# Performance work log

Measured on AMD Instinct MI355X. Metric: run time of the kernel, lower is better.

The kernel has to match this reference:

```python
import jax, jax.numpy as jnp
import numpy as np

N_NODES = 50000
N_EDGES = 800000
IN_FEATS, N_HIDDEN, N_CLASSES = 128, 128, 64
N_LAYERS = 3  # total GraphConv layers = N_LAYERS + 1


def setup_inputs() -> dict:
    key = jax.random.key(0)
    ks = jax.random.split(key, 16)
    features = jax.random.normal(ks[0], (N_NODES, IN_FEATS), dtype=jnp.float32)
    src = jax.random.randint(ks[1], (N_EDGES,), 0, N_NODES, dtype=jnp.int32)
    dst = jax.random.randint(ks[2], (N_EDGES,), 0, N_NODES, dtype=jnp.int32)
    def lin(k, fan_in, fan_out):
        s = 1.0 / np.sqrt(fan_in)
        return jax.random.uniform(k, (fan_in, fan_out), jnp.float32, -s, s)
    dims = [IN_FEATS] + [N_HIDDEN] * N_LAYERS + [N_CLASSES]
    inp = {"features": features, "src": src, "dst": dst}
    for i in range(len(dims) - 1):
        inp[f"W{i}"] = lin(ks[3 + i], dims[i], dims[i + 1])
        inp[f"b{i}"] = jnp.zeros((dims[i + 1],), jnp.float32)
    inp["Wp"] = lin(ks[10], N_CLASSES, 1)
    inp["bp"] = jnp.zeros((1,), jnp.float32)
    inp["Wv"] = lin(ks[11], N_CLASSES, 1)
    inp["bv"] = jnp.zeros((1,), jnp.float32)
    return inp


def _graph_conv(h, src, dst, norm_src, norm_dst, W, b, activate):
    # DGL GraphConv, norm='both': D_out^{-1/2} A D_in^{-1/2} X W + b
    h = h * norm_src  # [N, d]
    msg = h[src]      # [E, d] gather
    agg = jax.ops.segment_sum(msg, dst, num_segments=N_NODES)  # [N, d] scatter-add
    out = agg * norm_dst @ W + b
    return jax.nn.relu(out) if activate else out


def reference(features, src, dst, W0, b0, W1, b1, W2, b2, W3, b3, Wp, bp, Wv, bv):
    ones = jnp.ones((N_EDGES,), jnp.float32)
    out_deg = jax.ops.segment_sum(ones, src, num_segments=N_NODES)
    in_deg = jax.ops.segment_sum(ones, dst, num_segments=N_NODES)
    norm_src = jnp.clip(out_deg, 1.0) ** -0.5  # [N]
    norm_dst = jnp.clip(in_deg, 1.0) ** -0.5
    norm_src = norm_src[:, None]
    norm_dst = norm_dst[:, None]
    Ws = [W0, W1, W2, W3]
    bs = [b0, b1, b2, b3]
    h = features
    for i in range(4):
        h = _graph_conv(h, src, dst, norm_src, norm_dst, Ws[i], bs[i], activate=(i < 3))
    mN = jnp.sum(h, axis=0, keepdims=True)  # readout_nodes sum -> [1, n_classes]
    PI = h @ Wp + bp   # [N, 1]
    V = mN @ Wv + bv   # [1, 1]
    return (PI, V)
```

## Files before the change

### kernel.cpp

```cpp
#include <hip/hip_runtime.h>
#include <cstddef>

#define N_NODES 50000
#define N_EDGES 800000
#define NBUK    196
#define NBLK    256
#define EPB     3125
#define HEAD_BLOCKS 3136

typedef unsigned u32;
typedef unsigned short u16;
typedef unsigned char u8;
typedef __attribute__((ext_vector_type(8))) short bf16x8;
typedef __attribute__((ext_vector_type(4))) float f32x4;

__device__ __forceinline__ float bflo(u32 u) { return __uint_as_float(u << 16); }
__device__ __forceinline__ float bfhi(u32 u) { return __uint_as_float(u & 0xFFFF0000u); }
__device__ __forceinline__ u32 f2bf(float f) {
    u32 u = __float_as_uint(f);
    return (u + 0x7FFFu + ((u >> 16) & 1u)) >> 16;
}
__device__ __forceinline__ u32 packbf2(float a, float b) { return f2bf(a) | (f2bf(b) << 16); }

#define OFF_NS    0u
#define OFF_ND    200000u
#define OFF_RS    400000u
#define OFF_ES    600016u
#define OFF_CNTD  2200016u
#define OFF_CNTS  2400720u
#define OFF_TOTD  2601424u
#define OFF_TOTS  2602208u
#define OFF_BASED 2602992u
#define OFF_BASES 2603776u
#define OFF_VP    2604560u
#define OFF_DB    2617104u
#define OFF_SB    5817104u
#define OFF_T0    6617104u
#define OFF_T1    19417104u
#define OFF_TA    32217104u
#define OFF_TT    45017104u

__global__ __launch_bounds__(256)
void p1_kernel(const int* __restrict__ src, const int* __restrict__ dst,
               u32* __restrict__ cntD, u32* __restrict__ cntS) {
    __shared__ u32 dc[NBUK], sc[NBUK];
    int b = blockIdx.x, tid = threadIdx.x;
    if (tid < NBUK) { dc[tid] = 0; sc[tid] = 0; }
    __syncthreads();
    int lo = b * EPB, hi = lo + EPB;
    for (int e = lo + tid; e < hi; e += 256) {
        atomicAdd(&dc[dst[e] >> 8], 1u);
        atomicAdd(&sc[src[e] >> 8], 1u);
    }
    __syncthreads();
    if (tid < NBUK) {
        cntD[b * NBUK + tid] = dc[tid];
        cntS[b * NBUK + tid] = sc[tid];
    }
}

__global__ __launch_bounds__(256)
void p2a_kernel(u32* __restrict__ cntD, u32* __restrict__ cntS,
                u32* __restrict__ totD, u32* __restrict__ totS) {
    __shared__ u32 sc[256];
    int k = blockIdx.x, tid = threadIdx.x;
    u32 v = cntD[tid * NBUK + k];
    sc[tid] = v;
    __syncthreads();
    for (int o = 1; o < 256; o <<= 1) {
        u32 t = (tid >= o) ? sc[tid - o] : 0u;
        __syncthreads(); sc[tid] += t; __syncthreads();
    }
    cntD[tid * NBUK + k] = sc[tid] - v;
    if (tid == 255) totD[k] = sc[255];
    __syncthreads();
    v = cntS[tid * NBUK + k];
    sc[tid] = v;
    __syncthreads();
    for (int o = 1; o < 256; o <<= 1) {
        u32 t = (tid >= o) ? sc[tid - o] : 0u;
        __syncthreads(); sc[tid] += t; __syncthreads();
    }
    cntS[tid * NBUK + k] = sc[tid] - v;
    if (tid == 255) totS[k] = sc[255];
}

__global__ __launch_bounds__(256)
void p2b_kernel(const u32* __restrict__ totD, const u32* __restrict__ totS,
                u32* __restrict__ baseD, u32* __restrict__ baseS, u32* __restrict__ rs) {
    __shared__ u32 sc[256];
    int tid = threadIdx.x;
    u32 v = (tid < NBUK) ? totD[tid] : 0u;
    sc[tid] = v;
    __syncthreads();
    for (int o = 1; o < 256; o <<= 1) {
        u32 t = (tid >= o) ? sc[tid - o] : 0u;
        __syncthreads(); sc[tid] += t; __syncthreads();
    }
    if (tid < NBUK) baseD[tid] = sc[tid] - v;
    __syncthreads();
    v = (tid < NBUK) ? totS[tid] : 0u;
    sc[tid] = v;
    __syncthreads();
    for (int o = 1; o < 256; o <<= 1) {
        u32 t = (tid >= o) ? sc[tid - o] : 0u;
        __syncthreads(); sc[tid] += t; __syncthreads();
    }
    if (tid < NBUK) baseS[tid] = sc[tid] - v;
    if (tid == 0) rs[N_NODES] = N_EDGES;
}

__global__ __launch_bounds__(256)
void p3_kernel(const int* __restrict__ src, const int* __restrict__ dst,
               const u32* __restrict__ cntD, const u32* __restrict__ cntS,
               const u32* __restrict__ baseD, const u32* __restrict__ baseS,
               u32* __restrict__ db, u8* __restrict__ sb) {
    __shared__ u32 od[NBUK], os[NBUK];
    int b = blockIdx.x, tid = threadIdx.x;
    if (tid < NBUK) {
        od[tid] = baseD[tid] + cntD[b * NBUK + tid];
        os[tid] = baseS[tid] + cntS[b * NBUK + tid];
    }
    __syncthreads();
    int lo = b * EPB, hi = lo + EPB;
    for (int e = lo + tid; e < hi; e += 256) {
        int s = src[e], d = dst[e];
        u32 p = atomicAdd(&od[d >> 8], 1u);
        db[p] = ((u32)s << 8) | (u32)(d & 255);
        u32 q = atomicAdd(&os[s >> 8], 1u);
        sb[q] = (u8)(s & 255);
    }
}

__global__ __launch_bounds__(256)
void p4d_kernel(const u32* __restrict__ db, const u32* __restrict__ totD,
                const u32* __restrict__ baseD, float* __restrict__ nd,
                u32* __restrict__ rs, u16* __restrict__ es) {
    __shared__ u32 hist[256], sc[256], off[256];
    int k = blockIdx.x, tid = threadIdx.x;
    hist[tid] = 0;
    __syncthreads();
    u32 nEd = totD[k], base = baseD[k];
    for (u32 i = tid; i < nEd; i += 256)
        atomicAdd(&hist[db[base + i] & 255u], 1u);
    __syncthreads();
    u32 v = hist[tid];
    sc[tid] = v;
    __syncthreads();
    for (int o = 1; o < 256; o <<= 1) {
        u32 t = (tid >= o) ? sc[tid - o] : 0u;
        __syncthreads(); sc[tid] += t; __syncthreads();
    }
    u32 pf = sc[tid] - v;
    int node = k * 256 + tid;
    if (node < N_NODES) {
        rs[node] = base + pf;
        u32 c = v < 1u ? 1u : v;
        nd[node] = rsqrtf((float)c);
    }
    off[tid] = base + pf;
    __syncthreads();
    for (u32 i = tid; i < nEd; i += 256) {
        u32 p = db[base + i];
        u32 pos = atomicAdd(&off[p & 255u], 1u);
        es[pos] = (u16)(p >> 8);
    }
}

__global__ __launch_bounds__(256)
void p4sp_kernel(const u8* __restrict__ sb, const u32* __restrict__ totS,
                 const u32* __restrict__ baseS, float* __restrict__ ns,
                 const float* __restrict__ feat, u16* __restrict__ hS) {
    __shared__ u32 hist[256];
    __shared__ float sns[256];
    int k = blockIdx.x, tid = threadIdx.x;
    hist[tid] = 0;
    __syncthreads();
    u32 n = totS[k], base = baseS[k];
    for (u32 i = tid; i < n; i += 256)
        atomicAdd(&hist[sb[base + i]], 1u);
    __syncthreads();
    int node = k * 256 + tid;
    {
        u32 c = hist[tid]; if (c < 1u) c = 1u;
        float s = rsqrtf((float)c);
        sns[tid] = s;
        if (node < N_NODES) ns[node] = s;
    }
    __syncthreads();
    for (int i = tid; i < 256 * 32; i += 256) {
        int r = i >> 5, c4 = i & 31;
        int g = k * 256 + r;
        if (g >= N_NODES) break;
        float s = sns[r];
        float4 v = *(const float4*)&feat[(size_t)g * 128 + c4 * 4];
        uint2 o;
        o.x = packbf2(s * v.x, s * v.y);
        o.y = packbf2(s * v.z, s * v.w);
        *(uint2*)&hS[(size_t)g * 128 + c4 * 4] = o;
    }
}

__global__ __launch_bounds__(256)
void agg128_kernel(const u16* __restrict__ h, const u32* __restrict__ rs,
                   const u16* __restrict__ es, u16* __restrict__ agg) {
    int node = blockIdx.x * 4 + (threadIdx.x >> 6);
    int lane = threadIdx.x & 63;
    int quarter = lane >> 4;
    int q = lane & 15;
    const uint4* hp = (const uint4*)h;
    u32 s0 = rs[node], s1 = rs[node + 1];
    float acc[8] = {0.f, 0.f, 0.f, 0.f, 0.f, 0.f, 0.f, 0.f};
    u32 i = s0;
    for (; i + 16 <= s1; i += 16) {
        int e0 = es[i + quarter],     e1 = es[i + 4 + quarter];
        int e2 = es[i + 8 + quarter], e3 = es[i + 12 + quarter];
        uint4 a = hp[(size_t)e0 * 16 + q];
        uint4 b = hp[(size_t)e1 * 16 + q];
        uint4 c = hp[(size_t)e2 * 16 + q];
        uint4 d = hp[(size_t)e3 * 16 + q];
        acc[0] += (bflo(a.x) + bflo(b.x)) + (bflo(c.x) + bflo(d.x));
        acc[1] += (bfhi(a.x) + bfhi(b.x)) + (bfhi(c.x) + bfhi(d.x));
        acc[2] += (bflo(a.y) + bflo(b.y)) + (bflo(c.y) + bflo(d.y));
        acc[3] += (bfhi(a.y) + bfhi(b.y)) + (bfhi(c.y) + bfhi(d.y));
        acc[4] += (bflo(a.z) + bflo(b.z)) + (bflo(c.z) + bflo(d.z));
        acc[5] += (bfhi(a.z) + bfhi(b.z)) + (bfhi(c.z) + bfhi(d.z));
        acc[6] += (bflo(a.w) + bflo(b.w)) + (bflo(c.w) + bflo(d.w));
        acc[7] += (bfhi(a.w) + bfhi(b.w)) + (bfhi(c.w) + bfhi(d.w));
    }
    for (; i + 4 <= s1; i += 4) {
        uint4 a = hp[(size_t)es[i + quarter] * 16 + q];
        acc[0] += bflo(a.x); acc[1] += bfhi(a.x);
        acc[2] += bflo(a.y); acc[3] += bfhi(a.y);
        acc[4] += bflo(a.z); acc[5] += bfhi(a.z);
        acc[6] += bflo(a.w); acc[7] += bfhi(a.w);
    }
    u32 rem = s1 - i;
    if ((u32)quarter < rem) {
        uint4 a = hp[(size_t)es[i + quarter] * 16 + q];
        acc[0] += bflo(a.x); acc[1] += bfhi(a.x);
        acc[2] += bflo(a.y); acc[3] += bfhi(a.y);
        acc[4] += bflo(a.z); acc[5] += bfhi(a.z);
        acc[6] += bflo(a.w); acc[7] += bfhi(a.w);
    }
    #pragma unroll
    for (int j = 0; j < 8; ++j) {
        acc[j] += __shfl_xor(acc[j], 16, 64);
        acc[j] += __shfl_xor(acc[j], 32, 64);
    }
    if (lane < 16) {
        uint4 pk;
        pk.x = packbf2(acc[0], acc[1]);
        pk.y = packbf2(acc[2], acc[3]);
        pk.z = packbf2(acc[4], acc[5]);
        pk.w = packbf2(acc[6], acc[7]);
        *(uint4*)&agg[(size_t)node * 128 + q * 8] = pk;
    }
}

template <int NCOL, int MODE>
__global__ __launch_bounds__(256)
void mfma_gemm_kernel(const u16* __restrict__ Ab, const float* __restrict__ W,
                      const float* __restrict__ bias, const float* __restrict__ ns,
                      const float* __restrict__ nd, u16* __restrict__ C) {
    constexpr int NT = NCOL / 16;
    constexpr int WROW = 136;
    constexpr int CROW = NCOL + 4;
    __shared__ u16 Wt[NCOL * WROW];
    __shared__ float Cl[4][16 * CROW];
    int tid = threadIdx.x;
    int w = tid >> 6, lane = tid & 63;
    int rowbase = blockIdx.x * 64 + w * 16;

    for (int i = tid; i < 64 * NCOL; i += 256) {
        int k2 = i / NCOL, c = i % NCOL;
        float w0 = W[(size_t)(2 * k2) * NCOL + c];
        float w1 = W[(size_t)(2 * k2 + 1) * NCOL + c];
        *(u32*)&Wt[c * WROW + 2 * k2] = packbf2(w0, w1);
    }
    __syncthreads();

    int m = lane & 15, kb = lane >> 4;
    int arow = rowbase + m;
    if (arow > N_NODES - 1) arow = N_NODES - 1;
    f32x4 acc[NT];
    #pragma unroll
    for (int nt = 0; nt < NT; ++nt) acc[nt] = (f32x4){0.f, 0.f, 0.f, 0.f};

    #pragma unroll
    for (int ks = 0; ks < 4; ++ks) {
        int k0 = ks * 32 + kb * 8;
        bf16x8 a = *(const bf16x8*)&Ab[(size_t)arow * 128 + k0];
        #pragma unroll
        for (int nt = 0; nt < NT; ++nt) {
            bf16x8 b = *(const bf16x8*)&Wt[(nt * 16 + m) * WROW + k0];
            acc[nt] = __builtin_amdgcn_mfma_f32_16x16x32_bf16(a, b, acc[nt], 0, 0, 0);
        }
    }

    #pragma unroll
    for (int nt = 0; nt < NT; ++nt)
        #pragma unroll
        for (int reg = 0; reg < 4; ++reg)
            Cl[w][(kb * 4 + reg) * CROW + nt * 16 + m] = acc[nt][reg];
    __syncthreads();

    constexpr int CQ = NCOL / 4;
    for (int i = lane; i < 16 * CQ; i += 64) {
        int r = i / CQ, c4 = (i % CQ) * 4;
        int row = rowbase + r;
        if (row < N_NODES) {
            float4 o = *(float4*)&Cl[w][r * CROW + c4];
            if (MODE == 0) {
                float sd = nd[row], ss = ns[row];
                o.x = ss * fmaxf(sd * o.x + bias[c4 + 0], 0.f);
                o.y = ss * fmaxf(sd * o.y + bias[c4 + 1], 0.f);
                o.z = ss * fmaxf(sd * o.z + bias[c4 + 2], 0.f);
                o.w = ss * fmaxf(sd * o.w + bias[c4 + 3], 0.f);
            }
            uint2 pk = {packbf2(o.x, o.y), packbf2(o.z, o.w)};
            *(uint2*)&C[(size_t)row * NCOL + c4] = pk;
        }
    }
}

__global__ __launch_bounds__(256)
void l3head_kernel(const u16* __restrict__ t, const u32* __restrict__ rs,
                   const u16* __restrict__ es, const float* __restrict__ nd,
                   const float* __restrict__ b3, const float* __restrict__ Wp,
                   const float* __restrict__ Wv, const float* __restrict__ bp,
                   float* __restrict__ out, float* __restrict__ vpart) {
    __shared__ float sv;
    if (threadIdx.x == 0) sv = 0.f;
    __syncthreads();
    int lane = threadIdx.x & 63;
    int wvid = threadIdx.x >> 6;
    int oct = lane >> 3;
    int q = lane & 7;
    const uint4* hp = (const uint4*)t;
    float4 b3a = ((const float4*)b3)[q * 2];
    float4 b3b = ((const float4*)b3)[q * 2 + 1];
    float4 wpa = ((const float4*)Wp)[q * 2];
    float4 wpb = ((const float4*)Wp)[q * 2 + 1];
    float4 wva = ((const float4*)Wv)[q * 2];
    float4 wvb = ((const float4*)Wv)[q * 2 + 1];
    float bpv = bp[0];
    float vacc = 0.f;
    for (int n = blockIdx.x * 4 + wvid; n < N_NODES; n += HEAD_BLOCKS * 4) {
        u32 s0 = rs[n], s1 = rs[n + 1];
        float acc[8] = {0.f, 0.f, 0.f, 0.f, 0.f, 0.f, 0.f, 0.f};
        u32 i = s0;
        for (; i + 32 <= s1; i += 32) {
            int e0 = es[i + oct],      e1 = es[i + 8 + oct];
            int e2 = es[i + 16 + oct], e3 = es[i + 24 + oct];
            uint4 a = hp[(size_t)e0 * 8 + q];
            uint4 bb = hp[(size_t)e1 * 8 + q];
            uint4 c = hp[(size_t)e2 * 8 + q];
            uint4 d = hp[(size_t)e3 * 8 + q];
            acc[0] += (bflo(a.x) + bflo(bb.x)) + (bflo(c.x) + bflo(d.x));
            acc[1] += (bfhi(a.x) + bfhi(bb.x)) + (bfhi(c.x) + bfhi(d.x));
            acc[2] += (bflo(a.y) + bflo(bb.y)) + (bflo(c.y) + bflo(d.y));
            acc[3] += (bfhi(a.y) + bfhi(bb.y)) + (bfhi(c.y) + bfhi(d.y));
            acc[4] += (bflo(a.z) + bflo(bb.z)) + (bflo(c.z) + bflo(d.z));
            acc[5] += (bfhi(a.z) + bfhi(bb.z)) + (bfhi(c.z) + bfhi(d.z));
            acc[6] += (bflo(a.w) + bflo(bb.w)) + (bflo(c.w) + bflo(d.w));
            acc[7] += (bfhi(a.w) + bfhi(bb.w)) + (bfhi(c.w) + bfhi(d.w));
        }
        for (; i + 8 <= s1; i += 8) {
            uint4 a = hp[(size_t)es[i + oct] * 8 + q];
            acc[0] += bflo(a.x); acc[1] += bfhi(a.x);
            acc[2] += bflo(a.y); acc[3] += bfhi(a.y);
            acc[4] += bflo(a.z); acc[5] += bfhi(a.z);
            acc[6] += bflo(a.w); acc[7] += bfhi(a.w);
        }
        u32 rem = s1 - i;
        if ((u32)oct < rem) {
            uint4 a = hp[(size_t)es[i + oct] * 8 + q];
            acc[0] += bflo(a.x); acc[1] += bfhi(a.x);
            acc[2] += bflo(a.y); acc[3] += bfhi(a.y);
            acc[4] += bflo(a.z); acc[5] += bfhi(a.z);
            acc[6] += bflo(a.w); acc[7] += bfhi(a.w);
        }
        #pragma unroll
        for (int j = 0; j < 8; ++j) {
            acc[j] += __shfl_xor(acc[j], 8, 64);
            acc[j] += __shfl_xor(acc[j], 16, 64);
            acc[j] += __shfl_xor(acc[j], 32, 64);
        }
        float ndv = nd[n];
        float h0 = ndv * acc[0] + b3a.x, h1 = ndv * acc[1] + b3a.y;
        float h2 = ndv * acc[2] + b3a.z, h3 = ndv * acc[3] + b3a.w;
        float h4 = ndv * acc[4] + b3b.x, h5 = ndv * acc[5] + b3b.y;
        float h6 = ndv * acc[6] + b3b.z, h7 = ndv * acc[7] + b3b.w;
        float p  = h0 * wpa.x + h1 * wpa.y + h2 * wpa.z + h3 * wpa.w
                 + h4 * wpb.x + h5 * wpb.y + h6 * wpb.z + h7 * wpb.w;
        float vv = h0 * wva.x + h1 * wva.y + h2 * wva.z + h3 * wva.w
                 + h4 * wvb.x + h5 * wvb.y + h6 * wvb.z + h7 * wvb.w;
        p  += __shfl_xor(p, 1, 64);  p  += __shfl_xor(p, 2, 64);  p  += __shfl_xor(p, 4, 64);
        vv += __shfl_xor(vv, 1, 64); vv += __shfl_xor(vv, 2, 64); vv += __shfl_xor(vv, 4, 64);
        if (lane == 0) { out[n] = p + bpv; vacc += vv; }
    }
    if (lane == 0) atomicAdd(&sv, vacc);
    __syncthreads();
    if (threadIdx.x == 0) vpart[blockIdx.x] = sv;
}

__global__ __launch_bounds__(256)
void vred_kernel(const float* __restrict__ vpart, const float* __restrict__ bv,
                 float* __restrict__ out) {
    float v = 0.f;
    for (int i = threadIdx.x; i < HEAD_BLOCKS; i += 256) v += vpart[i];
    #pragma unroll
    for (int off = 32; off; off >>= 1) v += __shfl_down(v, off, 64);
    __shared__ float s[4];
    if ((threadIdx.x & 63) == 0) s[threadIdx.x >> 6] = v;
    __syncthreads();
    if (threadIdx.x == 0) out[N_NODES] = s[0] + s[1] + s[2] + s[3] + bv[0];
}

extern "C" void kernel_launch(void* const* d_in, const int* in_sizes, int n_in,
                              void* d_out, int out_size, void* d_ws, size_t ws_size,
                              hipStream_t stream) {
    const float* feat = (const float*)d_in[0];
    const int*   src  = (const int*)d_in[1];
    const int*   dst  = (const int*)d_in[2];
    const float* W0 = (const float*)d_in[3];  const float* b0 = (const float*)d_in[4];
    const float* W1 = (const float*)d_in[5];  const float* b1 = (const float*)d_in[6];
    const float* W2 = (const float*)d_in[7];  const float* b2 = (const float*)d_in[8];
    const float* W3 = (const float*)d_in[9];  const float* b3 = (const float*)d_in[10];
    const float* Wp = (const float*)d_in[11]; const float* bp = (const float*)d_in[12];
    const float* Wv = (const float*)d_in[13]; const float* bv = (const float*)d_in[14];
    float* out = (float*)d_out;
    char*  wsb = (char*)d_ws;

    float* ns    = (float*)(wsb + OFF_NS);
    float* nd    = (float*)(wsb + OFF_ND);
    u32*   rs    = (u32*)(wsb + OFF_RS);
    u16*   es    = (u16*)(wsb + OFF_ES);
    u32*   cntD  = (u32*)(wsb + OFF_CNTD);
    u32*   cntS  = (u32*)(wsb + OFF_CNTS);
    u32*   totD  = (u32*)(wsb + OFF_TOTD);
    u32*   totS  = (u32*)(wsb + OFF_TOTS);
    u32*   baseD = (u32*)(wsb + OFF_BASED);
    u32*   baseS = (u32*)(wsb + OFF_BASES);
    float* vpart = (float*)(wsb + OFF_VP);
    u32*   db    = (u32*)(wsb + OFF_DB);
    u8*    sb    = (u8*)(wsb + OFF_SB);
    u16*   T0    = (u16*)(wsb + OFF_T0);
    u16*   T1    = (u16*)(wsb + OFF_T1);
    u16*   TA    = (u16*)(wsb + OFF_TA);
    u16*   Tt    = (u16*)(wsb + OFF_TT);

    p1_kernel<<<NBLK, 256, 0, stream>>>(src, dst, cntD, cntS);
    p2a_kernel<<<NBUK, 256, 0, stream>>>(cntD, cntS, totD, totS);
    p2b_kernel<<<1, 256, 0, stream>>>(totD, totS, baseD, baseS, rs);
    p3_kernel<<<NBLK, 256, 0, stream>>>(src, dst, cntD, cntS, baseD, baseS, db, sb);
    p4d_kernel<<<NBUK, 256, 0, stream>>>(db, totD, baseD, nd, rs, es);
    p4sp_kernel<<<NBUK, 256, 0, stream>>>(sb, totS, baseS, ns, feat, T0);

    agg128_kernel<<<12500, 256, 0, stream>>>(T0, rs, es, TA);
    mfma_gemm_kernel<128, 0><<<782, 256, 0, stream>>>(TA, W0, b0, ns, nd, T1);
    agg128_kernel<<<12500, 256, 0, stream>>>(T1, rs, es, TA);
    mfma_gemm_kernel<128, 0><<<782, 256, 0, stream>>>(TA, W1, b1, ns, nd, T0);
    agg128_kernel<<<12500, 256, 0, stream>>>(T0, rs, es, TA);
    mfma_gemm_kernel<128, 0><<<782, 256, 0, stream>>>(TA, W2, b2, ns, nd, T1);
    mfma_gemm_kernel<64, 1><<<782, 256, 0, stream>>>(T1, W3, b3, ns, nd, Tt);
    l3head_kernel<<<HEAD_BLOCKS, 256, 0, stream>>>(Tt, rs, es, nd, b3, Wp, Wv, bp, out, vpart);
    vred_kernel<<<1, 256, 0, stream>>>(vpart, bv, out);
}
```

Measured before the change: 355.1 us.

## Fuse neighbor aggregation with MFMA GEMM and pre-convert weights once

Merges the per-layer aggregation and GEMM kernels into one kernel. Each block aggregates 32 node rows into shared memory and then multiplies them by the weights with MFMA. Weights are converted to bf16 and transposed once in a new upfront kernel and read straight from global memory, instead of being repacked into LDS by every GEMM block. This removes the bf16 round-trip of the aggregated tensor through global memory and three kernel launches. In exchange, each wave now processes 8 nodes serially, which lowers the parallelism available to hide gather latency, and every block re-reads the weight fragments from global/L2.

```diff
diff --git a/kernel.cpp b/kernel.cpp
--- a/kernel.cpp
+++ b/kernel.cpp
@@ -37,8 +37,9 @@
 #define OFF_SB    5817104u
 #define OFF_T0    6617104u
 #define OFF_T1    19417104u
-#define OFF_TA    32217104u
+#define OFF_T2    32217104u
 #define OFF_TT    45017104u
+#define OFF_WT    51417104u
 
 __global__ __launch_bounds__(256)
 void p1_kernel(const int* __restrict__ src, const int* __restrict__ dst,
@@ -202,124 +203,155 @@
 }
 
 __global__ __launch_bounds__(256)
-void agg128_kernel(const u16* __restrict__ h, const u32* __restrict__ rs,
-                   const u16* __restrict__ es, u16* __restrict__ agg) {
-    int node = blockIdx.x * 4 + (threadIdx.x >> 6);
-    int lane = threadIdx.x & 63;
-    int quarter = lane >> 4;
-    int q = lane & 15;
-    const uint4* hp = (const uint4*)h;
-    u32 s0 = rs[node], s1 = rs[node + 1];
-    float acc[8] = {0.f, 0.f, 0.f, 0.f, 0.f, 0.f, 0.f, 0.f};
-    u32 i = s0;
-    for (; i + 16 <= s1; i += 16) {
-        int e0 = es[i + quarter],     e1 = es[i + 4 + quarter];
-        int e2 = es[i + 8 + quarter], e3 = es[i + 12 + quarter];
-        uint4 a = hp[(size_t)e0 * 16 + q];
-        uint4 b = hp[(size_t)e1 * 16 + q];
-        uint4 c = hp[(size_t)e2 * 16 + q];
-        uint4 d = hp[(size_t)e3 * 16 + q];
-        acc[0] += (bflo(a.x) + bflo(b.x)) + (bflo(c.x) + bflo(d.x));
-        acc[1] += (bfhi(a.x) + bfhi(b.x)) + (bfhi(c.x) + bfhi(d.x));
-        acc[2] += (bflo(a.y) + bflo(b.y)) + (bflo(c.y) + bflo(d.y));
-        acc[3] += (bfhi(a.y) + bfhi(b.y)) + (bfhi(c.y) + bfhi(d.y));
-        acc[4] += (bflo(a.z) + bflo(b.z)) + (bflo(c.z) + bflo(d.z));
-        acc[5] += (bfhi(a.z) + bfhi(b.z)) + (bfhi(c.z) + bfhi(d.z));
-        acc[6] += (bflo(a.w) + bflo(b.w)) + (bflo(c.w) + bflo(d.w));
-        acc[7] += (bfhi(a.w) + bfhi(b.w)) + (bfhi(c.w) + bfhi(d.w));
-    }
-    for (; i + 4 <= s1; i += 4) {
-        uint4 a = hp[(size_t)es[i + quarter] * 16 + q];
-        acc[0] += bflo(a.x); acc[1] += bfhi(a.x);
-        acc[2] += bflo(a.y); acc[3] += bfhi(a.y);
-        acc[4] += bflo(a.z); acc[5] += bfhi(a.z);
-        acc[6] += bflo(a.w); acc[7] += bfhi(a.w);
-    }
-    u32 rem = s1 - i;
-    if ((u32)quarter < rem) {
-        uint4 a = hp[(size_t)es[i + quarter] * 16 + q];
-        acc[0] += bflo(a.x); acc[1] += bfhi(a.x);
-        acc[2] += bflo(a.y); acc[3] += bfhi(a.y);
-        acc[4] += bflo(a.z); acc[5] += bfhi(a.z);
-        acc[6] += bflo(a.w); acc[7] += bfhi(a.w);
-    }
-    #pragma unroll
-    for (int j = 0; j < 8; ++j) {
-        acc[j] += __shfl_xor(acc[j], 16, 64);
-        acc[j] += __shfl_xor(acc[j], 32, 64);
-    }
-    if (lane < 16) {
-        uint4 pk;
-        pk.x = packbf2(acc[0], acc[1]);
-        pk.y = packbf2(acc[2], acc[3]);
-        pk.z = packbf2(acc[4], acc[5]);
-        pk.w = packbf2(acc[6], acc[7]);
-        *(uint4*)&agg[(size_t)node * 128 + q * 8] = pk;
-    }
-}
-
-template <int NCOL, int MODE>
-__global__ __launch_bounds__(256)
-void mfma_gemm_kernel(const u16* __restrict__ Ab, const float* __restrict__ W,
-                      const float* __restrict__ bias, const float* __restrict__ ns,
-                      const float* __restrict__ nd, u16* __restrict__ C) {
-    constexpr int NT = NCOL / 16;
-    constexpr int WROW = 136;
-    constexpr int CROW = NCOL + 4;
-    __shared__ u16 Wt[NCOL * WROW];
-    __shared__ float Cl[4][16 * CROW];
+void wconv_kernel(const float* __restrict__ W0, const float* __restrict__ W1,
+                  const float* __restrict__ W2, const float* __restrict__ W3,
+                  u16* __restrict__ wt) {
+    int i = blockIdx.x * 256 + threadIdx.x;
+    if (i < 49152) {
+        int l = i / 16384, r = i % 16384;
+        int c = r >> 7, k = r & 127;
+        const float* W = (l == 0) ? W0 : (l == 1) ? W1 : W2;
+        wt[l * 16384 + r] = (u16)f2bf(W[k * 128 + c]);
+    } else if (i < 49152 + 8192) {
+        int r = i - 49152;
+        int c = r >> 7, k = r & 127;
+        wt[49152 + r] = (u16)f2bf(W3[k * 64 + c]);
+    }
+}
+
+__global__ __launch_bounds__(256)
+void aggmm_kernel(const u16* __restrict__ h, const u32* __restrict__ rs,
+                  const u16* __restrict__ es, const u16* __restrict__ wt,
+                  const float* __restrict__ bias, const float* __restrict__ ns,
+                  const float* __restrict__ nd, u16* __restrict__ C) {
+    __shared__ u16 As[32 * 136];
     int tid = threadIdx.x;
     int w = tid >> 6, lane = tid & 63;
-    int rowbase = blockIdx.x * 64 + w * 16;
-
-    for (int i = tid; i < 64 * NCOL; i += 256) {
-        int k2 = i / NCOL, c = i % NCOL;
-        float w0 = W[(size_t)(2 * k2) * NCOL + c];
-        float w1 = W[(size_t)(2 * k2 + 1) * NCOL + c];
-        *(u32*)&Wt[c * WROW + 2 * k2] = packbf2(w0, w1);
+    int quarter = lane >> 4, q = lane & 15;
+    int rowbase = blockIdx.x * 32;
+    const uint4* hp = (const uint4*)h;
+
+    for (int j = 0; j < 8; ++j) {
+        int lr = w * 8 + j;
+        int node = rowbase + lr;
+        float acc[8] = {0.f, 0.f, 0.f, 0.f, 0.f, 0.f, 0.f, 0.f};
+        if (node < N_NODES) {
+            u32 s0 = rs[node], s1 = rs[node + 1];
+            u32 i = s0;
+            for (; i + 16 <= s1; i += 16) {
+                int e0 = es[i + quarter],     e1 = es[i + 4 + quarter];
+                int e2 = es[i + 8 + quarter], e3 = es[i + 12 + quarter];
+                uint4 a = hp[(size_t)e0 * 16 + q];
+                uint4 b = hp[(size_t)e1 * 16 + q];
+                uint4 c = hp[(size_t)e2 * 16 + q];
+                uint4 d = hp[(size_t)e3 * 16 + q];
+                acc[0] += (bflo(a.x) + bflo(b.x)) + (bflo(c.x) + bflo(d.x));
+                acc[1] += (bfhi(a.x) + bfhi(b.x)) + (bfhi(c.x) + bfhi(d.x));
+                acc[2] += (bflo(a.y) + bflo(b.y)) + (bflo(c.y) + bflo(d.y));
+                acc[3] += (bfhi(a.y) + bfhi(b.y)) + (bfhi(c.y) + bfhi(d.y));
+                acc[4] += (bflo(a.z) + bflo(b.z)) + (bflo(c.z) + bflo(d.z));
+                acc[5] += (bfhi(a.z) + bfhi(b.z)) + (bfhi(c.z) + bfhi(d.z));
+                acc[6] += (bflo(a.w) + bflo(b.w)) + (bflo(c.w) + bflo(d.w));
+                acc[7] += (bfhi(a.w) + bfhi(b.w)) + (bfhi(c.w) + bfhi(d.w));
+            }
+            for (; i + 4 <= s1; i += 4) {
+                uint4 a = hp[(size_t)es[i + quarter] * 16 + q];
+                acc[0] += bflo(a.x); acc[1] += bfhi(a.x);
+                acc[2] += bflo(a.y); acc[3] += bfhi(a.y);
+                acc[4] += bflo(a.z); acc[5] += bfhi(a.z);
+                acc[6] += bflo(a.w); acc[7] += bfhi(a.w);
+            }
+            u32 rem = s1 - i;
+            if ((u32)quarter < rem) {
+                uint4 a = hp[(size_t)es[i + quarter] * 16 + q];
+                acc[0] += bflo(a.x); acc[1] += bfhi(a.x);
+                acc[2] += bflo(a.y); acc[3] += bfhi(a.y);
+                acc[4] += bflo(a.z); acc[5] += bfhi(a.z);
+                acc[6] += bflo(a.w); acc[7] += bfhi(a.w);
+            }
+        }
+        #pragma unroll
+        for (int jj = 0; jj < 8; ++jj) {
+            acc[jj] += __shfl_xor(acc[jj], 16, 64);
+            acc[jj] += __shfl_xor(acc[jj], 32, 64);
+        }
+        if (lane < 16) {
+            uint4 pk;
+            pk.x = packbf2(acc[0], acc[1]);
+            pk.y = packbf2(acc[2], acc[3]);
+            pk.z = packbf2(acc[4], acc[5]);
+            pk.w = packbf2(acc[6], acc[7]);
+            *(uint4*)&As[lr * 136 + q * 8] = pk;
+        }
     }
     __syncthreads();
 
     int m = lane & 15, kb = lane >> 4;
-    int arow = rowbase + m;
-    if (arow > N_NODES - 1) arow = N_NODES - 1;
-    f32x4 acc[NT];
+    int mtile = w >> 1, nhalf = w & 1;
+    f32x4 acc[4];
     #pragma unroll
-    for (int nt = 0; nt < NT; ++nt) acc[nt] = (f32x4){0.f, 0.f, 0.f, 0.f};
-
+    for (int nt = 0; nt < 4; ++nt) acc[nt] = (f32x4){0.f, 0.f, 0.f, 0.f};
     #pragma unroll
     for (int ks = 0; ks < 4; ++ks) {
         int k0 = ks * 32 + kb * 8;
-        bf16x8 a = *(const bf16x8*)&Ab[(size_t)arow * 128 + k0];
+        bf16x8 a = *(const bf16x8*)&As[(mtile * 16 + m) * 136 + k0];
         #pragma unroll
-        for (int nt = 0; nt < NT; ++nt) {
-            bf16x8 b = *(const bf16x8*)&Wt[(nt * 16 + m) * WROW + k0];
+        for (int nt = 0; nt < 4; ++nt) {
+            int c = nhalf * 64 + nt * 16 + m;
+            bf16x8 b = *(const bf16x8*)&wt[(size_t)c * 128 + k0];
             acc[nt] = __builtin_amdgcn_mfma_f32_16x16x32_bf16(a, b, acc[nt], 0, 0, 0);
         }
     }
-
     #pragma unroll
-    for (int nt = 0; nt < NT; ++nt)
+    for (int nt = 0; nt < 4; ++nt) {
+        int c = nhalf * 64 + nt * 16 + m;
+        float bs = bias[c];
         #pragma unroll
-        for (int reg = 0; reg < 4; ++reg)
-            Cl[w][(kb * 4 + reg) * CROW + nt * 16 + m] = acc[nt][reg];
-    __syncthreads();
-
-    constexpr int CQ = NCOL / 4;
-    for (int i = lane; i < 16 * CQ; i += 64) {
-        int r = i / CQ, c4 = (i % CQ) * 4;
-        int row = rowbase + r;
-        if (row < N_NODES) {
-            float4 o = *(float4*)&Cl[w][r * CROW + c4];
-            if (MODE == 0) {
-                float sd = nd[row], ss = ns[row];
-                o.x = ss * fmaxf(sd * o.x + bias[c4 + 0], 0.f);
-                o.y = ss * fmaxf(sd * o.y + bias[c4 + 1], 0.f);
-                o.z = ss * fmaxf(sd * o.z + bias[c4 + 2], 0.f);
-                o.w = ss * fmaxf(sd * o.w + bias[c4 + 3], 0.f);
-            }
-            uint2 pk = {packbf2(o.x, o.y), packbf2(o.z, o.w)};
-            *(uint2*)&C[(size_t)row * NCOL + c4] = pk;
+        for (int reg = 0; reg < 4; ++reg) {
+            int row = rowbase + mtile * 16 + kb * 4 + reg;
+            int rc = row < N_NODES ? row : N_NODES - 1;
+            float o = ns[rc] * fmaxf(nd[rc] * acc[nt][reg] + bs, 0.f);
+            float o2 = __shfl_xor(o, 1, 64);
+            if (!(m & 1) && row < N_NODES)
+                *(u32*)&C[(size_t)row * 128 + c] = packbf2(o, o2);
+        }
+    }
+}
+
+__global__ __launch_bounds__(256)
+void tf64_kernel(const u16* __restrict__ Ain, const u16* __restrict__ wt,
+                 u16* __restrict__ Cout) {
+    int tid = threadIdx.x;
+    int w = tid >> 6, lane = tid & 63;
+    int m = lane & 15, kb = lane >> 4;
+    int mtile = w >> 1, nhalf = w & 1;
+    int rowbase = blockIdx.x * 32;
+    int arow = rowbase + mtile * 16 + m;
+    if (arow > N_NODES - 1) arow = N_NODES - 1;
+    f32x4 acc[2];
+    acc[0] = (f32x4){0.f, 0.f, 0.f, 0.f};
+    acc[1] = (f32x4){0.f, 0.f, 0.f, 0.f};
+    #pragma unroll
+    for (int ks = 0; ks < 4; ++ks) {
+        int k0 = ks * 32 + kb * 8;
+        bf16x8 a = *(const bf16x8*)&Ain[(size_t)arow * 128 + k0];
+        #pragma unroll
+        for (int nt = 0; nt < 2; ++nt) {
+            int c = nhalf * 32 + nt * 16 + m;
+            bf16x8 b = *(const bf16x8*)&wt[(size_t)c * 128 + k0];
+            acc[nt] = __builtin_amdgcn_mfma_f32_16x16x32_bf16(a, b, acc[nt], 0, 0, 0);
+        }
+    }
+    #pragma unroll
+    for (int nt = 0; nt < 2; ++nt) {
+        int c = nhalf * 32 + nt * 16 + m;
+        #pragma unroll
+        for (int reg = 0; reg < 4; ++reg) {
+            int row = rowbase + mtile * 16 + kb * 4 + reg;
+            float o = acc[nt][reg];
+            float o2 = __shfl_xor(o, 1, 64);
+            if (!(m & 1) && row < N_NODES)
+                *(u32*)&Cout[(size_t)row * 64 + c] = packbf2(o, o2);
         }
     }
 }
@@ -448,9 +480,11 @@
     u8*    sb    = (u8*)(wsb + OFF_SB);
     u16*   T0    = (u16*)(wsb + OFF_T0);
     u16*   T1    = (u16*)(wsb + OFF_T1);
-    u16*   TA    = (u16*)(wsb + OFF_TA);
+    u16*   T2    = (u16*)(wsb + OFF_T2);
     u16*   Tt    = (u16*)(wsb + OFF_TT);
-
+    u16*   wt    = (u16*)(wsb + OFF_WT);
+
+    wconv_kernel<<<224, 256, 0, stream>>>(W0, W1, W2, W3, wt);
     p1_kernel<<<NBLK, 256, 0, stream>>>(src, dst, cntD, cntS);
     p2a_kernel<<<NBUK, 256, 0, stream>>>(cntD, cntS, totD, totS);
     p2b_kernel<<<1, 256, 0, stream>>>(totD, totS, baseD, baseS, rs);
@@ -458,13 +492,10 @@
     p4d_kernel<<<NBUK, 256, 0, stream>>>(db, totD, baseD, nd, rs, es);
     p4sp_kernel<<<NBUK, 256, 0, stream>>>(sb, totS, baseS, ns, feat, T0);
 
-    agg128_kernel<<<12500, 256, 0, stream>>>(T0, rs, es, TA);
-    mfma_gemm_kernel<128, 0><<<782, 256, 0, stream>>>(TA, W0, b0, ns, nd, T1);
-    agg128_kernel<<<12500, 256, 0, stream>>>(T1, rs, es, TA);
-    mfma_gemm_kernel<128, 0><<<782, 256, 0, stream>>>(TA, W1, b1, ns, nd, T0);
-    agg128_kernel<<<12500, 256, 0, stream>>>(T0, rs, es, TA);
-    mfma_gemm_kernel<128, 0><<<782, 256, 0, stream>>>(TA, W2, b2, ns, nd, T1);
-    mfma_gemm_kernel<64, 1><<<782, 256, 0, stream>>>(T1, W3, b3, ns, nd, Tt);
+    aggmm_kernel<<<1563, 256, 0, stream>>>(T0, rs, es, wt,          b0, ns, nd, T1);
+    aggmm_kernel<<<1563, 256, 0, stream>>>(T1, rs, es, wt + 16384,  b1, ns, nd, T2);
+    aggmm_kernel<<<1563, 256, 0, stream>>>(T2, rs, es, wt + 32768,  b2, ns, nd, T0);
+    tf64_kernel<<<1563, 256, 0, stream>>>(T0, wt + 49152, Tt);
     l3head_kernel<<<HEAD_BLOCKS, 256, 0, stream>>>(Tt, rs, es, nd, b3, Wp, Wv, bp, out, vpart);
     vred_kernel<<<1, 256, 0, stream>>>(vpart, bv, out);
 }
```

New measurement: 396.5 us. 11.7% more time.
